# Performance work log

Hardware: AMD Instinct MI355X
Metric: run time of the kernel (lower is better)

## Reference

```python
import jax, jax.numpy as jnp
import numpy as np

T, H, E, I, K = 4096, 1024, 8, 1024, 2  # tokens, hidden, experts, intermediate, top_k


def setup_inputs() -> dict:
    key = jax.random.key(0)
    k1, k2, k3, k4, k5 = jax.random.split(key, 5)
    x = jax.random.normal(k1, (T, H), dtype=jnp.float32)
    router_logits = jax.random.normal(k2, (T, E), dtype=jnp.float32)
    per_expert_scale = jnp.ones((E,), dtype=jnp.float32)
    # FusedMoE layout: w13 = fused [gate; up] projection [E, 2I, H], w2 = down [E, H, I]
    w13 = jax.random.normal(k3, (E, 2 * I, H), dtype=jnp.float32) * 0.02
    w2 = jax.random.normal(k4, (E, H, I), dtype=jnp.float32) * 0.02
    return {"x": x, "router_logits": router_logits,
            "per_expert_scale": per_expert_scale, "w13": w13, "w2": w2}


def reference(x, router_logits, per_expert_scale, w13, w2):
    # --- Gemma4 routing: softmax over ALL experts -> top-k -> renormalize ---
    _, topk_ids = jax.lax.top_k(router_logits, K)              # [T, K] int32
    probs = jax.nn.softmax(router_logits, axis=-1)             # [T, E]
    indicator = jax.nn.one_hot(topk_ids, E, dtype=probs.dtype).sum(axis=-2)  # [T, E]
    gate = indicator * probs
    renorm = gate.sum(axis=-1, keepdims=True)
    renorm = jnp.where(renorm > 0.0, renorm, 1.0)
    dispatch = gate / renorm                                   # zero off top-k
    # per_expert_scale folded into routing weights (only top-k slots nonzero)
    combine_w = dispatch * per_expert_scale[None, :]           # [T, E]

    # --- expert FFN (gelu gate * up -> down), combined with routing weights ---
    w1, w3 = w13[:, :I, :], w13[:, I:, :]                      # [E, I, H] each
    g = jnp.einsum('th,eih->tei', x, w1)                       # gate proj
    u = jnp.einsum('th,eih->tei', x, w3)                       # up proj
    h = jax.nn.gelu(g, approximate=False) * u                  # exact GELU (torch default)
    y = jnp.einsum('tei,ehi->teh', h, w2)                      # down proj
    out = jnp.einsum('te,teh->th', combine_w, y)               # weighted combine
    return out
```

## Files before the change

### kernel.cpp

```cpp
#include <hip/hip_runtime.h>
#include <hip/hip_bf16.h>

#define T_TOK 4096
#define H_DIM 1024
#define E_NUM 8
#define I_DIM 1024
#define PAD_CAP 9216
#define RBLK 16

typedef __attribute__((ext_vector_type(4))) float f32x4;
typedef __attribute__((ext_vector_type(8))) short bf16x8;

__device__ __forceinline__ unsigned short f2b(float f) {
  union { float f; unsigned int u; } v; v.f = f;
  unsigned int r = v.u + 0x7fffu + ((v.u >> 16) & 1u);
  return (unsigned short)(r >> 16);
}

__device__ __forceinline__ void async_copy16(const void* g, void* l) {
  __builtin_amdgcn_global_load_lds(
      (const __attribute__((address_space(1))) void*)g,
      (__attribute__((address_space(3))) void*)l, 16, 0, 0);
}

__global__ __launch_bounds__(256) void k_prep(
    const float* __restrict__ x, const float* __restrict__ logits,
    const float* __restrict__ scale,
    const float* __restrict__ w13, const float* __restrict__ w2,
    unsigned short* __restrict__ xb, unsigned short* __restrict__ w13b,
    unsigned short* __restrict__ w2b,
    int* __restrict__ tids, float* __restrict__ cw, int* __restrict__ cnt) {
  const int b = blockIdx.x;
  if (b < RBLK) {
    __shared__ int s_cnt[E_NUM];
    const int tid = threadIdx.x;
    if (tid < E_NUM) s_cnt[tid] = 0;
    __syncthreads();
    int t = b * 256 + tid;
    float l[E_NUM];
    *(float4*)(l)     = *(const float4*)(logits + (size_t)t * E_NUM);
    *(float4*)(l + 4) = *(const float4*)(logits + (size_t)t * E_NUM + 4);
    float m = l[0];
#pragma unroll
    for (int i = 1; i < E_NUM; ++i) m = fmaxf(m, l[i]);
    float p[E_NUM]; float s = 0.f;
#pragma unroll
    for (int i = 0; i < E_NUM; ++i) { p[i] = expf(l[i] - m); s += p[i]; }
    int i0 = 0; float b0 = l[0];
#pragma unroll
    for (int i = 1; i < E_NUM; ++i) if (l[i] > b0) { b0 = l[i]; i0 = i; }
    int i1 = -1; float b1 = -1e30f;
#pragma unroll
    for (int i = 0; i < E_NUM; ++i) if (i != i0 && l[i] > b1) { b1 = l[i]; i1 = i; }
    float g0 = p[i0] / s, g1 = p[i1] / s;
    float r = g0 + g1;
    cw[t * 2]     = g0 / r * scale[i0];
    cw[t * 2 + 1] = g1 / r * scale[i1];
    tids[t * 2] = i0; tids[t * 2 + 1] = i1;
    atomicAdd(&s_cnt[i0], 1);
    atomicAdd(&s_cnt[i1], 1);
    __syncthreads();
    if (tid < E_NUM) cnt[b * E_NUM + tid] = s_cnt[tid];
    return;
  }
  const int cb = b - RBLK;
  const float* src; unsigned short* dst; size_t base;
  if (cb < 2048)       { src = x;   dst = xb;   base = (size_t)cb * 2048; }
  else if (cb < 10240) { src = w13; dst = w13b; base = (size_t)(cb - 2048) * 2048; }
  else                 { src = w2;  dst = w2b;  base = (size_t)(cb - 10240) * 2048; }
  size_t i = base + (size_t)threadIdx.x * 8;
  float4 f0 = *(const float4*)(src + i);
  float4 f1 = *(const float4*)(src + i + 4);
  uint4 pk;
  pk.x = (unsigned)f2b(f0.x) | ((unsigned)f2b(f0.y) << 16);
  pk.y = (unsigned)f2b(f0.z) | ((unsigned)f2b(f0.w) << 16);
  pk.z = (unsigned)f2b(f1.x) | ((unsigned)f2b(f1.y) << 16);
  pk.w = (unsigned)f2b(f1.z) | ((unsigned)f2b(f1.w) << 16);
  *(uint4*)(dst + i) = pk;
}

__global__ __launch_bounds__(256) void k_scan(
    const int* __restrict__ cnt, int* __restrict__ pad_off,
    int* __restrict__ base, int* __restrict__ perm) {
  __shared__ int s_tot[E_NUM], s_off[E_NUM + 1];
  const int tid = threadIdx.x;
  if (tid == 0) {
    int off = 0;
    for (int e = 0; e < E_NUM; ++e) {
      int tot = 0;
      for (int b = 0; b < RBLK; ++b) tot += cnt[b * E_NUM + e];
      s_tot[e] = tot;
      s_off[e] = off; pad_off[e] = off;
      int run = off;
      for (int b = 0; b < RBLK; ++b) { base[b * E_NUM + e] = run; run += cnt[b * E_NUM + e]; }
      off += (tot + 127) & ~127;
    }
    s_off[E_NUM] = off; pad_off[E_NUM] = off;
  }
  __syncthreads();
  for (int e = 0; e < E_NUM; ++e) {
    int start = s_off[e] + s_tot[e];
    int end   = s_off[e + 1];
    for (int i = start + tid; i < end; i += 256) perm[i] = -1;
  }
}

__global__ __launch_bounds__(256) void k_scatter(
    const int* __restrict__ tids, const int* __restrict__ base,
    int* __restrict__ perm, int* __restrict__ inv) {
  __shared__ int l_cnt[E_NUM];
  const int b = blockIdx.x, tid = threadIdx.x;
  if (tid < E_NUM) l_cnt[tid] = 0;
  __syncthreads();
  int t = b * 256 + tid;
  int i0 = tids[t * 2], i1 = tids[t * 2 + 1];
  int r0 = atomicAdd(&l_cnt[i0], 1);
  int s0 = base[b * E_NUM + i0] + r0;
  perm[s0] = t * 2; inv[t * 2] = s0;
  int r1 = atomicAdd(&l_cnt[i1], 1);
  int s1 = base[b * E_NUM + i1] + r1;
  perm[s1] = t * 2 + 1; inv[t * 2 + 1] = s1;
}

__global__ __launch_bounds__(256, 2) void k_gemm1(
    const unsigned short* __restrict__ xbf,
    const unsigned short* __restrict__ w13b,
    const int* __restrict__ perm, const int* __restrict__ pad_off,
    unsigned short* __restrict__ h_buf) {
  __shared__ __align__(16) unsigned short a_lds[128 * 64];
  __shared__ __align__(16) unsigned short b_lds[128 * 64];
  const int tid = threadIdx.x;
  const int wave = tid >> 6, lane = tid & 63;
  const int row0 = blockIdx.y * 128;
  if (row0 >= pad_off[E_NUM]) return;
  int e = 0;
#pragma unroll
  for (int i = 1; i < E_NUM; ++i) if (row0 >= pad_off[i]) e = i;
  const int iBase = blockIdx.x * 64;

  const int srcChunk = (lane & 7) ^ ((lane >> 3) & 7);

  const unsigned short* agbase[4];
#pragma unroll
  for (int j = 0; j < 4; ++j) {
    int r = j * 32 + wave * 8 + (lane >> 3);
    int p = perm[row0 + r];
    int tok = (p < 0) ? 0 : (p >> 1);
    agbase[j] = xbf + (size_t)tok * H_DIM + srcChunk * 8;
  }
  const unsigned short* bgbase[4];
#pragma unroll
  for (int j = 0; j < 4; ++j) {
    int brow = j * 32 + wave * 8 + (lane >> 3);
    int seg = brow >> 5, half = seg & 1;
    int col = iBase + (seg >> 1) * 32 + (brow & 31);
    bgbase[j] = w13b + ((size_t)e * 2 * I_DIM + half * I_DIM + col) * H_DIM + srcChunk * 8;
  }

  f32x4 acc[4][4];
#pragma unroll
  for (int mi = 0; mi < 4; ++mi)
#pragma unroll
    for (int ni = 0; ni < 4; ++ni) acc[mi][ni] = (f32x4)(0.f);

  const int wm = wave >> 1, wn = wave & 1;
  const int ml = lane & 15, quad = lane >> 4;

  for (int k0 = 0; k0 < H_DIM; k0 += 64) {
    __syncthreads();
#pragma unroll
    for (int j = 0; j < 4; ++j)
      async_copy16(agbase[j] + k0, a_lds + (j * 256 + wave * 64) * 8);
#pragma unroll
    for (int j = 0; j < 4; ++j)
      async_copy16(bgbase[j] + k0, b_lds + (j * 256 + wave * 64) * 8);
    __syncthreads();
#pragma unroll
    for (int ks = 0; ks < 2; ++ks) {
      const int ch = ((ks * 4 + quad) ^ (ml & 7)) * 8;
      bf16x8 af[4], bfr[4];
#pragma unroll
      for (int mi = 0; mi < 4; ++mi)
        af[mi] = *(const bf16x8*)(a_lds + (wm * 64 + mi * 16 + ml) * 64 + ch);
#pragma unroll
      for (int ni = 0; ni < 4; ++ni)
        bfr[ni] = *(const bf16x8*)(b_lds + (wn * 64 + ni * 16 + ml) * 64 + ch);
#pragma unroll
      for (int mi = 0; mi < 4; ++mi)
#pragma unroll
        for (int ni = 0; ni < 4; ++ni)
          acc[mi][ni] = __builtin_amdgcn_mfma_f32_16x16x32_bf16(af[mi], bfr[ni], acc[mi][ni], 0, 0, 0);
    }
  }
#pragma unroll
  for (int mi = 0; mi < 4; ++mi) {
#pragma unroll
    for (int nc = 0; nc < 2; ++nc) {
      f32x4 g = acc[mi][nc];
      f32x4 uu = acc[mi][nc + 2];
#pragma unroll
      for (int r = 0; r < 4; ++r) {
        int row = row0 + wm * 64 + mi * 16 + quad * 4 + r;
        int col = iBase + wn * 32 + nc * 16 + ml;
        float gg = g[r];
        float hv = 0.5f * gg * (1.f + erff(gg * 0.7071067811865475f)) * uu[r];
        h_buf[(size_t)row * I_DIM + col] = f2b(hv);
      }
    }
  }
}

__global__ __launch_bounds__(256, 2) void k_gemm2(
    const unsigned short* __restrict__ h_buf,
    const unsigned short* __restrict__ w2b,
    const int* __restrict__ pad_off,
    unsigned short* __restrict__ y) {
  __shared__ __align__(16) unsigned short a_lds[128 * 64];
  __shared__ __align__(16) unsigned short b_lds[64 * 64];
  const int tid = threadIdx.x;
  const int wave = tid >> 6, lane = tid & 63;
  const int row0 = blockIdx.y * 128;
  if (row0 >= pad_off[E_NUM]) return;
  int e = 0;
#pragma unroll
  for (int i = 1; i < E_NUM; ++i) if (row0 >= pad_off[i]) e = i;
  const int cBase = blockIdx.x * 64;
  const int srcChunk = (lane & 7) ^ ((lane >> 3) & 7);

  const unsigned short* agbase[4];
#pragma unroll
  for (int j = 0; j < 4; ++j) {
    int r = j * 32 + wave * 8 + (lane >> 3);
    agbase[j] = h_buf + (size_t)(row0 + r) * I_DIM + srcChunk * 8;
  }
  const unsigned short* bgbase[2];
#pragma unroll
  for (int j = 0; j < 2; ++j) {
    int brow = j * 32 + wave * 8 + (lane >> 3);
    bgbase[j] = w2b + ((size_t)e * H_DIM + cBase + brow) * I_DIM + srcChunk * 8;
  }
  f32x4 acc[2][4];
#pragma unroll
  for (int mi = 0; mi < 2; ++mi)
#pragma unroll
    for (int ni = 0; ni < 4; ++ni) acc[mi][ni] = (f32x4)(0.f);
  const int ml = lane & 15, quad = lane >> 4;

  for (int k0 = 0; k0 < I_DIM; k0 += 64) {
    __syncthreads();
#pragma unroll
    for (int j = 0; j < 4; ++j)
      async_copy16(agbase[j] + k0, a_lds + (j * 256 + wave * 64) * 8);
#pragma unroll
    for (int j = 0; j < 2; ++j)
      async_copy16(bgbase[j] + k0, b_lds + (j * 256 + wave * 64) * 8);
    __syncthreads();
#pragma unroll
    for (int ks = 0; ks < 2; ++ks) {
      const int ch = ((ks * 4 + quad) ^ (ml & 7)) * 8;
      bf16x8 af[2], bfr[4];
#pragma unroll
      for (int mi = 0; mi < 2; ++mi)
        af[mi] = *(const bf16x8*)(a_lds + (wave * 32 + mi * 16 + ml) * 64 + ch);
#pragma unroll
      for (int ni = 0; ni < 4; ++ni)
        bfr[ni] = *(const bf16x8*)(b_lds + (ni * 16 + ml) * 64 + ch);
#pragma unroll
      for (int mi = 0; mi < 2; ++mi)
#pragma unroll
        for (int ni = 0; ni < 4; ++ni)
          acc[mi][ni] = __builtin_amdgcn_mfma_f32_16x16x32_bf16(af[mi], bfr[ni], acc[mi][ni], 0, 0, 0);
    }
  }
#pragma unroll
  for (int mi = 0; mi < 2; ++mi) {
#pragma unroll
    for (int ni = 0; ni < 4; ++ni) {
#pragma unroll
      for (int r = 0; r < 4; ++r) {
        int row = row0 + wave * 32 + mi * 16 + quad * 4 + r;
        int col = cBase + ni * 16 + ml;
        y[(size_t)row * H_DIM + col] = f2b(acc[mi][ni][r]);
      }
    }
  }
}

__global__ void k_combine(const unsigned short* __restrict__ y,
                          const int* __restrict__ inv, const float* __restrict__ cw,
                          float* __restrict__ out) {
  const int t = blockIdx.x;
  const int c = threadIdx.x * 4;
  int s0 = inv[t * 2], s1 = inv[t * 2 + 1];
  float c0 = cw[t * 2], c1 = cw[t * 2 + 1];
  uint2 a = *(const uint2*)(y + (size_t)s0 * H_DIM + c);
  uint2 b = *(const uint2*)(y + (size_t)s1 * H_DIM + c);
  union { unsigned v; float f; } w;
  float4 o;
  float alo, ahi, blo, bhi;
  w.v = a.x << 16;          alo = w.f;
  w.v = a.x & 0xffff0000u;  ahi = w.f;
  w.v = b.x << 16;          blo = w.f;
  w.v = b.x & 0xffff0000u;  bhi = w.f;
  o.x = c0 * alo + c1 * blo;
  o.y = c0 * ahi + c1 * bhi;
  w.v = a.y << 16;          alo = w.f;
  w.v = a.y & 0xffff0000u;  ahi = w.f;
  w.v = b.y << 16;          blo = w.f;
  w.v = b.y & 0xffff0000u;  bhi = w.f;
  o.z = c0 * alo + c1 * blo;
  o.w = c0 * ahi + c1 * bhi;
  *(float4*)(out + (size_t)t * H_DIM + c) = o;
}

extern "C" void kernel_launch(void* const* d_in, const int* in_sizes, int n_in,
                              void* d_out, int out_size, void* d_ws, size_t ws_size,
                              hipStream_t stream) {
  const float* x      = (const float*)d_in[0];
  const float* logits = (const float*)d_in[1];
  const float* scale  = (const float*)d_in[2];
  const float* w13    = (const float*)d_in[3];
  const float* w2     = (const float*)d_in[4];
  float* out = (float*)d_out;

  char* ws = (char*)d_ws;
  int*   pad_off = (int*)(ws + 128);
  int*   cnt     = (int*)(ws + 1024);
  int*   base    = (int*)(ws + 2048);
  int*   tids    = (int*)(ws + 4096);
  float* cw      = (float*)(ws + 65536);
  int*   perm    = (int*)(ws + 131072);
  int*   inv     = (int*)(ws + 196608);
  unsigned short* xb    = (unsigned short*)(ws + 0x40000);
  unsigned short* h_buf = (unsigned short*)(ws + 0x900000);
  unsigned short* w13b  = (unsigned short*)(ws + 0x1C00000);
  unsigned short* ybuf  = w13b;
  unsigned short* w2b   = (unsigned short*)(ws + 0x3C00000);

  k_prep<<<14336 + RBLK, 256, 0, stream>>>(x, logits, scale, w13, w2,
                                           xb, w13b, w2b, tids, cw, cnt);
  k_scan<<<1, 256, 0, stream>>>(cnt, pad_off, base, perm);
  k_scatter<<<RBLK, 256, 0, stream>>>(tids, base, perm, inv);
  k_gemm1<<<dim3(16, PAD_CAP / 128), 256, 0, stream>>>(xb, w13b, perm, pad_off, h_buf);
  k_gemm2<<<dim3(16, PAD_CAP / 128), 256, 0, stream>>>(h_buf, w2b, pad_off, ybuf);
  k_combine<<<T_TOK, 256, 0, stream>>>(ybuf, inv, cw, out);
}
```

Measured before the change: 241.8 us.

## Fuse weighted combine into down-proj GEMM epilogue via atomics; merge scan into scatter

```diff
diff --git a/kernel.cpp b/kernel.cpp
--- a/kernel.cpp
+++ b/kernel.cpp
@@ -7,6 +7,8 @@
 #define I_DIM 1024
 #define PAD_CAP 9216
 #define RBLK 16
+#define CONVB 14336
+#define ZEROB 2048
 
 typedef __attribute__((ext_vector_type(4))) float f32x4;
 typedef __attribute__((ext_vector_type(8))) short bf16x8;
@@ -29,11 +31,12 @@
     const float* __restrict__ w13, const float* __restrict__ w2,
     unsigned short* __restrict__ xb, unsigned short* __restrict__ w13b,
     unsigned short* __restrict__ w2b,
-    int* __restrict__ tids, float* __restrict__ cw, int* __restrict__ cnt) {
+    int* __restrict__ tids, float* __restrict__ cw, int* __restrict__ cnt,
+    float* __restrict__ out) {
   const int b = blockIdx.x;
+  const int tid = threadIdx.x;
   if (b < RBLK) {
     __shared__ int s_cnt[E_NUM];
-    const int tid = threadIdx.x;
     if (tid < E_NUM) s_cnt[tid] = 0;
     __syncthreads();
     int t = b * 256 + tid;
@@ -63,63 +66,71 @@
     if (tid < E_NUM) cnt[b * E_NUM + tid] = s_cnt[tid];
     return;
   }
-  const int cb = b - RBLK;
-  const float* src; unsigned short* dst; size_t base;
-  if (cb < 2048)       { src = x;   dst = xb;   base = (size_t)cb * 2048; }
-  else if (cb < 10240) { src = w13; dst = w13b; base = (size_t)(cb - 2048) * 2048; }
-  else                 { src = w2;  dst = w2b;  base = (size_t)(cb - 10240) * 2048; }
-  size_t i = base + (size_t)threadIdx.x * 8;
-  float4 f0 = *(const float4*)(src + i);
-  float4 f1 = *(const float4*)(src + i + 4);
-  uint4 pk;
-  pk.x = (unsigned)f2b(f0.x) | ((unsigned)f2b(f0.y) << 16);
-  pk.y = (unsigned)f2b(f0.z) | ((unsigned)f2b(f0.w) << 16);
-  pk.z = (unsigned)f2b(f1.x) | ((unsigned)f2b(f1.y) << 16);
-  pk.w = (unsigned)f2b(f1.z) | ((unsigned)f2b(f1.w) << 16);
-  *(uint4*)(dst + i) = pk;
-}
-
-__global__ __launch_bounds__(256) void k_scan(
-    const int* __restrict__ cnt, int* __restrict__ pad_off,
-    int* __restrict__ base, int* __restrict__ perm) {
-  __shared__ int s_tot[E_NUM], s_off[E_NUM + 1];
-  const int tid = threadIdx.x;
+  if (b < RBLK + CONVB) {
+    const int cb = b - RBLK;
+    const float* src; unsigned short* dst; size_t base;
+    if (cb < 2048)       { src = x;   dst = xb;   base = (size_t)cb * 2048; }
+    else if (cb < 10240) { src = w13; dst = w13b; base = (size_t)(cb - 2048) * 2048; }
+    else                 { src = w2;  dst = w2b;  base = (size_t)(cb - 10240) * 2048; }
+    size_t i = base + (size_t)tid * 8;
+    float4 f0 = *(const float4*)(src + i);
+    float4 f1 = *(const float4*)(src + i + 4);
+    uint4 pk;
+    pk.x = (unsigned)f2b(f0.x) | ((unsigned)f2b(f0.y) << 16);
+    pk.y = (unsigned)f2b(f0.z) | ((unsigned)f2b(f0.w) << 16);
+    pk.z = (unsigned)f2b(f1.x) | ((unsigned)f2b(f1.y) << 16);
+    pk.w = (unsigned)f2b(f1.z) | ((unsigned)f2b(f1.w) << 16);
+    *(uint4*)(dst + i) = pk;
+    return;
+  }
+  const int zb = b - RBLK - CONVB;
+  size_t i = (size_t)zb * 2048 + (size_t)tid * 8;
+  float4 z = {0.f, 0.f, 0.f, 0.f};
+  *(float4*)(out + i) = z;
+  *(float4*)(out + i + 4) = z;
+}
+
+__global__ __launch_bounds__(256) void k_scatter16(
+    const int* __restrict__ cnt, const int* __restrict__ tids,
+    int* __restrict__ pad_off, int* __restrict__ perm, int* __restrict__ inv) {
+  __shared__ int l_cnt[E_NUM];
+  __shared__ int s_base[E_NUM];
+  __shared__ int s_off[E_NUM + 1], s_tot[E_NUM];
+  const int b = blockIdx.x, tid = threadIdx.x;
+  if (tid < E_NUM) l_cnt[tid] = 0;
   if (tid == 0) {
     int off = 0;
     for (int e = 0; e < E_NUM; ++e) {
-      int tot = 0;
-      for (int b = 0; b < RBLK; ++b) tot += cnt[b * E_NUM + e];
+      int tot = 0, mine = 0;
+      for (int k = 0; k < RBLK; ++k) {
+        if (k == b) mine = tot;
+        tot += cnt[k * E_NUM + e];
+      }
       s_tot[e] = tot;
-      s_off[e] = off; pad_off[e] = off;
-      int run = off;
-      for (int b = 0; b < RBLK; ++b) { base[b * E_NUM + e] = run; run += cnt[b * E_NUM + e]; }
+      s_off[e] = off;
+      s_base[e] = off + mine;
       off += (tot + 127) & ~127;
     }
-    s_off[E_NUM] = off; pad_off[E_NUM] = off;
-  }
-  __syncthreads();
-  for (int e = 0; e < E_NUM; ++e) {
-    int start = s_off[e] + s_tot[e];
-    int end   = s_off[e + 1];
-    for (int i = start + tid; i < end; i += 256) perm[i] = -1;
-  }
-}
-
-__global__ __launch_bounds__(256) void k_scatter(
-    const int* __restrict__ tids, const int* __restrict__ base,
-    int* __restrict__ perm, int* __restrict__ inv) {
-  __shared__ int l_cnt[E_NUM];
-  const int b = blockIdx.x, tid = threadIdx.x;
-  if (tid < E_NUM) l_cnt[tid] = 0;
+    s_off[E_NUM] = off;
+    if (b == 0) {
+      for (int e = 0; e <= E_NUM; ++e) pad_off[e] = s_off[e];
+    }
+  }
   __syncthreads();
   int t = b * 256 + tid;
   int i0 = tids[t * 2], i1 = tids[t * 2 + 1];
   int r0 = atomicAdd(&l_cnt[i0], 1);
-  int s0 = base[b * E_NUM + i0] + r0;
+  int s0 = s_base[i0] + r0;
   perm[s0] = t * 2; inv[t * 2] = s0;
   int r1 = atomicAdd(&l_cnt[i1], 1);
-  int s1 = base[b * E_NUM + i1] + r1;
+  int s1 = s_base[i1] + r1;
   perm[s1] = t * 2 + 1; inv[t * 2 + 1] = s1;
+  int gid = b * 256 + tid;
+  for (int e = 0; e < E_NUM; ++e) {
+    int start = s_off[e] + s_tot[e];
+    int end   = s_off[e + 1];
+    for (int i = start + gid; i < end; i += RBLK * 256) perm[i] = -1;
+  }
 }
 
 __global__ __launch_bounds__(256, 2) void k_gemm1(
@@ -213,10 +224,12 @@
 __global__ __launch_bounds__(256, 2) void k_gemm2(
     const unsigned short* __restrict__ h_buf,
     const unsigned short* __restrict__ w2b,
-    const int* __restrict__ pad_off,
-    unsigned short* __restrict__ y) {
+    const int* __restrict__ perm, const int* __restrict__ pad_off,
+    const float* __restrict__ cw, float* __restrict__ out) {
   __shared__ __align__(16) unsigned short a_lds[128 * 64];
   __shared__ __align__(16) unsigned short b_lds[64 * 64];
+  __shared__ int s_tok[128];
+  __shared__ float s_cw[128];
   const int tid = threadIdx.x;
   const int wave = tid >> 6, lane = tid & 63;
   const int row0 = blockIdx.y * 128;
@@ -225,6 +238,11 @@
 #pragma unroll
   for (int i = 1; i < E_NUM; ++i) if (row0 >= pad_off[i]) e = i;
   const int cBase = blockIdx.x * 64;
+  if (tid < 128) {
+    int p = perm[row0 + tid];
+    s_tok[tid] = (p < 0) ? -1 : (p >> 1);
+    s_cw[tid] = (p < 0) ? 0.f : cw[p];
+  }
   const int srcChunk = (lane & 7) ^ ((lane >> 3) & 7);
 
   const unsigned short* agbase[4];
@@ -278,39 +296,14 @@
     for (int ni = 0; ni < 4; ++ni) {
 #pragma unroll
       for (int r = 0; r < 4; ++r) {
-        int row = row0 + wave * 32 + mi * 16 + quad * 4 + r;
-        int col = cBase + ni * 16 + ml;
-        y[(size_t)row * H_DIM + col] = f2b(acc[mi][ni][r]);
+        int lrow = wave * 32 + mi * 16 + quad * 4 + r;
+        int tok = s_tok[lrow];
+        if (tok >= 0)
+          atomicAdd(&out[(size_t)tok * H_DIM + cBase + ni * 16 + ml],
+                    s_cw[lrow] * acc[mi][ni][r]);
       }
     }
   }
-}
-
-__global__ void k_combine(const unsigned short* __restrict__ y,
-                          const int* __restrict__ inv, const float* __restrict__ cw,
-                          float* __restrict__ out) {
-  const int t = blockIdx.x;
-  const int c = threadIdx.x * 4;
-  int s0 = inv[t * 2], s1 = inv[t * 2 + 1];
-  float c0 = cw[t * 2], c1 = cw[t * 2 + 1];
-  uint2 a = *(const uint2*)(y + (size_t)s0 * H_DIM + c);
-  uint2 b = *(const uint2*)(y + (size_t)s1 * H_DIM + c);
-  union { unsigned v; float f; } w;
-  float4 o;
-  float alo, ahi, blo, bhi;
-  w.v = a.x << 16;          alo = w.f;
-  w.v = a.x & 0xffff0000u;  ahi = w.f;
-  w.v = b.x << 16;          blo = w.f;
-  w.v = b.x & 0xffff0000u;  bhi = w.f;
-  o.x = c0 * alo + c1 * blo;
-  o.y = c0 * ahi + c1 * bhi;
-  w.v = a.y << 16;          alo = w.f;
-  w.v = a.y & 0xffff0000u;  ahi = w.f;
-  w.v = b.y << 16;          blo = w.f;
-  w.v = b.y & 0xffff0000u;  bhi = w.f;
-  o.z = c0 * alo + c1 * blo;
-  o.w = c0 * ahi + c1 * bhi;
-  *(float4*)(out + (size_t)t * H_DIM + c) = o;
 }
 
 extern "C" void kernel_launch(void* const* d_in, const int* in_sizes, int n_in,
@@ -326,7 +319,6 @@
   char* ws = (char*)d_ws;
   int*   pad_off = (int*)(ws + 128);
   int*   cnt     = (int*)(ws + 1024);
-  int*   base    = (int*)(ws + 2048);
   int*   tids    = (int*)(ws + 4096);
   float* cw      = (float*)(ws + 65536);
   int*   perm    = (int*)(ws + 131072);
@@ -334,14 +326,11 @@
   unsigned short* xb    = (unsigned short*)(ws + 0x40000);
   unsigned short* h_buf = (unsigned short*)(ws + 0x900000);
   unsigned short* w13b  = (unsigned short*)(ws + 0x1C00000);
-  unsigned short* ybuf  = w13b;
   unsigned short* w2b   = (unsigned short*)(ws + 0x3C00000);
 
-  k_prep<<<14336 + RBLK, 256, 0, stream>>>(x, logits, scale, w13, w2,
-                                           xb, w13b, w2b, tids, cw, cnt);
-  k_scan<<<1, 256, 0, stream>>>(cnt, pad_off, base, perm);
-  k_scatter<<<RBLK, 256, 0, stream>>>(tids, base, perm, inv);
+  k_prep<<<RBLK + CONVB + ZEROB, 256, 0, stream>>>(x, logits, scale, w13, w2,
+                                                   xb, w13b, w2b, tids, cw, cnt, out);
+  k_scatter16<<<RBLK, 256, 0, stream>>>(cnt, tids, pad_off, perm, inv);
   k_gemm1<<<dim3(16, PAD_CAP / 128), 256, 0, stream>>>(xb, w13b, perm, pad_off, h_buf);
-  k_gemm2<<<dim3(16, PAD_CAP / 128), 256, 0, stream>>>(h_buf, w2b, pad_off, ybuf);
-  k_combine<<<T_TOK, 256, 0, stream>>>(ybuf, inv, cw, out);
-}
+  k_gemm2<<<dim3(16, PAD_CAP / 128), 256, 0, stream>>>(h_buf, w2b, perm, pad_off, cw, out);
+}
```

Measured after the change: 250.6 us. 3.6% more time.
